# Performance work log

Hardware: AMD Instinct MI355X
Metric: run time of the kernel (lower is better)

## Reference

```python
import jax, jax.numpy as jnp
import numpy as np

SEQ, BATCH, D_IN, D_H, RANK, D_OUT = 512, 128, 256, 1024, 128, 256


def setup_inputs() -> dict:
    key = jax.random.key(0)
    ks = jax.random.split(key, 7)
    s = 1.0 / np.sqrt(D_H)
    return {
        "x": jax.random.normal(ks[0], (SEQ, BATCH, D_IN), jnp.float32),
        "W_in": jax.random.normal(ks[1], (D_H, D_IN), jnp.float32) * (1.0 / np.sqrt(D_IN)),
        "U": jax.random.uniform(ks[2], (RANK, D_H), jnp.float32, -s, s),
        "V": jax.random.uniform(ks[3], (D_H, RANK), jnp.float32, -s, s),
        "b_h": jax.random.uniform(ks[4], (D_H,), jnp.float32, -s, s),
        "W_out": jax.random.normal(ks[5], (D_OUT, D_H), jnp.float32) * (1.0 / np.sqrt(D_H)),
        "b_out": jax.random.uniform(ks[6], (D_OUT,), jnp.float32, -s, s),
    }


def reference(x, W_in, U, V, b_h, W_out, b_out):
    # Precompute input projection for all timesteps: i2h has no bias (bias=0).
    zi = jnp.einsum('tbi,hi->tbh', x, W_in)  # [T,B,H]

    def step(h, zi_t):
        # low-rank h2h: h @ (V@U)^T + b_h == (h @ U^T) @ V^T + b_h
        zh = (h @ U.T) @ V.T + b_h
        h_new = jax.nn.relu(zh + zi_t)
        return h_new, h_new

    h0 = jnp.zeros((x.shape[1], V.shape[0]), x.dtype)
    _, hidden = jax.lax.scan(step, h0, zi)  # [T,B,H]
    output = hidden @ W_out.T + b_out       # [T,B,O]; output_activation=None -> identity
    return hidden, output
```

## Files before the change

### kernel.cpp

```cpp
#include <hip/hip_runtime.h>

typedef __bf16 bf16;
typedef __bf16 bf16x4 __attribute__((ext_vector_type(4)));
typedef __bf16 bf16x8 __attribute__((ext_vector_type(8)));
typedef float  f32x4  __attribute__((ext_vector_type(4)));
typedef unsigned long long u64;

#define MFMA(a,b,c) __builtin_amdgcn_mfma_f32_16x16x32_bf16((a),(b),(c),0,0,0)

#define TSTEPS 512
#define NBATCH 128
#define DIN    256
#define DH     1024
#define NRANK  128
#define DOUT   256

#define NBG 8
#define NGH 4

#define ZI_OFF    0ull
#define QSEQ_OFF  134217728ull
#define PBUF_OFF  150994944ull
#define FLAG_OFF  (PBUF_OFF + 262144ull)
#define WIN_OFF   151519232ull
#define U_OFF     152043520ull
#define V_OFF     152305664ull
#define WOUT_OFF  152567808ull
#define BAR_OFF   153092096ull

__device__ __forceinline__ void cstore64(u64* p, u64 v) {
  __hip_atomic_store(p, v, __ATOMIC_RELAXED, __HIP_MEMORY_SCOPE_AGENT);
}
__device__ __forceinline__ u64 cload64(const u64* p) {
  return __hip_atomic_load(p, __ATOMIC_RELAXED, __HIP_MEMORY_SCOPE_AGENT);
}
union B4U { u64 u; bf16x4 b; };

__global__ __launch_bounds__(256) void k_prep(const float* __restrict__ W_in,
                                              const float* __restrict__ U,
                                              const float* __restrict__ V,
                                              const float* __restrict__ W_out,
                                              char* __restrict__ ws) {
  bf16* winb  = (bf16*)(ws + WIN_OFF);
  bf16* ub    = (bf16*)(ws + U_OFF);
  bf16* vb    = (bf16*)(ws + V_OFF);
  bf16* woutb = (bf16*)(ws + WOUT_OFF);
  bf16* qseq  = (bf16*)(ws + QSEQ_OFF);
  unsigned* flg = (unsigned*)(ws + FLAG_OFF);
  size_t id = (size_t)blockIdx.x * 256 + threadIdx.x;
  if      (id < 262144) winb[id]           = (bf16)W_in[id];
  else if (id < 393216) ub[id - 262144]    = (bf16)U[id - 262144];
  else if (id < 524288) vb[id - 393216]    = (bf16)V[id - 393216];
  else if (id < 786432) woutb[id - 524288] = (bf16)W_out[id - 524288];
  else if (id < 802816) qseq[id - 786432]  = (bf16)0.0f;
  else if (id < 802848) flg[id - 802816]   = 0u;
}

__global__ __launch_bounds__(256) void k_zi(const float* __restrict__ x,
                                            const char* __restrict__ ws,
                                            bf16* __restrict__ zi) {
  const bf16* winb = (const bf16*)(ws + WIN_OFF);
  __shared__ bf16 xl[128 * 264];
  __shared__ bf16 wl[128 * 264];
  const int tid = threadIdx.x, lane = tid & 63, wv = tid >> 6;
  const int q4 = lane >> 4, l16 = lane & 15;
  const int m0b = blockIdx.x * 128, n0 = blockIdx.y * 128;

  for (int ch = tid; ch < 8192; ch += 256) {
    int r = ch >> 6, c4 = ch & 63;
    float4 f = *(const float4*)&x[(size_t)(m0b + r) * 256 + c4 * 4];
    bf16x4 b; b[0] = (bf16)f.x; b[1] = (bf16)f.y; b[2] = (bf16)f.z; b[3] = (bf16)f.w;
    *(bf16x4*)&xl[r * 264 + c4 * 4] = b;
  }
  for (int ch = tid; ch < 4096; ch += 256) {
    int r = ch >> 5, c8 = ch & 31;
    *(uint4*)&wl[r * 264 + c8 * 8] = *(const uint4*)&winb[(size_t)(n0 + r) * 256 + c8 * 8];
  }
  __syncthreads();

  f32x4 z4 = {0.f, 0.f, 0.f, 0.f};
  f32x4 acc[2][8];
#pragma unroll
  for (int i = 0; i < 2; i++)
#pragma unroll
    for (int j = 0; j < 8; j++) acc[i][j] = z4;

  const int m0 = wv * 32;
#pragma unroll
  for (int kc = 0; kc < 8; kc++) {
    bf16x8 a0 = *(bf16x8*)&xl[(m0 + l16) * 264 + kc * 32 + q4 * 8];
    bf16x8 a1 = *(bf16x8*)&xl[(m0 + 16 + l16) * 264 + kc * 32 + q4 * 8];
#pragma unroll
    for (int nt = 0; nt < 8; nt++) {
      bf16x8 b = *(bf16x8*)&wl[(nt * 16 + l16) * 264 + kc * 32 + q4 * 8];
      acc[0][nt] = MFMA(a0, b, acc[0][nt]);
      acc[1][nt] = MFMA(a1, b, acc[1][nt]);
    }
  }
  __syncthreads();
#pragma unroll
  for (int mt = 0; mt < 2; mt++)
#pragma unroll
    for (int nt = 0; nt < 8; nt++)
#pragma unroll
      for (int r = 0; r < 4; r++) {
        int m = m0 + mt * 16 + q4 * 4 + r;
        int c = nt * 16 + l16;
        xl[m * 136 + c] = (bf16)acc[mt][nt][r];
      }
  __syncthreads();
  for (int ch = tid; ch < 2048; ch += 256) {
    int r = ch >> 4, c8 = ch & 15;
    *(uint4*)&zi[(size_t)(m0b + r) * 1024 + n0 + c8 * 8] = *(uint4*)&xl[r * 136 + c8 * 8];
  }
}

__global__ __launch_bounds__(256) void k_scan(char* __restrict__ ws,
                                              const float* __restrict__ b_h) {
  const bf16* zi = (const bf16*)(ws + ZI_OFF);
  const bf16* ub = (const bf16*)(ws + U_OFF);
  const bf16* vb = (const bf16*)(ws + V_OFF);
  bf16* qseq = (bf16*)(ws + QSEQ_OFF);
  u64* pbufq = (u64*)(ws + PBUF_OFF);
  unsigned* flag = (unsigned*)(ws + FLAG_OFF);

  __shared__ bf16 Vl[256 * 136];
  __shared__ bf16 Ul[128 * 264];
  __shared__ bf16 ql[16 * 136];
  __shared__ bf16 hl[16 * 264];
  __shared__ bf16 ps[16 * 136];

  const int tid = threadIdx.x, lane = tid & 63, w = tid >> 6;
  const int l16 = lane & 15, q4 = lane >> 4;
  const int bg = blockIdx.x & 7, g = blockIdx.x >> 3;
  const int brow0 = bg * 16, hcol0 = g * 256;

  for (int ch = tid; ch < 4096; ch += 256) {
    int r = ch >> 4, c8 = ch & 15;
    *(uint4*)&Vl[r * 136 + c8 * 8] = *(const uint4*)&vb[(size_t)(hcol0 + r) * 128 + c8 * 8];
  }
  for (int ch = tid; ch < 4096; ch += 256) {
    int r = ch >> 5, c8 = ch & 31;
    *(uint4*)&Ul[r * 264 + c8 * 8] = *(const uint4*)&ub[(size_t)r * 1024 + hcol0 + c8 * 8];
  }
  for (int i = tid; i < 16 * 136; i += 256) ql[i] = (bf16)0.0f;

  float bj[4];
#pragma unroll
  for (int nt = 0; nt < 4; nt++) bj[nt] = b_h[hcol0 + w * 64 + nt * 16 + l16];

  bf16 zcur[16], znxt[16];
#pragma unroll
  for (int nt = 0; nt < 4; nt++)
#pragma unroll
    for (int rr = 0; rr < 4; rr++)
      zcur[nt * 4 + rr] = zi[(size_t)(brow0 + q4 * 4 + rr) * 1024 + hcol0 + w * 64 + nt * 16 + l16];
  __syncthreads();

  const f32x4 z4 = {0.f, 0.f, 0.f, 0.f};

  for (int t = 0; t < TSTEPS - 1; t++) {
    f32x4 az[4] = {z4, z4, z4, z4};
#pragma unroll
    for (int kc = 0; kc < 4; kc++) {
      bf16x8 a = *(const bf16x8*)&ql[l16 * 136 + kc * 32 + q4 * 8];
#pragma unroll
      for (int nt = 0; nt < 4; nt++) {
        bf16x8 bb = *(const bf16x8*)&Vl[(w * 64 + nt * 16 + l16) * 136 + kc * 32 + q4 * 8];
        az[nt] = MFMA(a, bb, az[nt]);
      }
    }
#pragma unroll
    for (int nt = 0; nt < 4; nt++)
#pragma unroll
      for (int rr = 0; rr < 4; rr++) {
        float v = az[nt][rr] + bj[nt] + (float)zcur[nt * 4 + rr];
        hl[(q4 * 4 + rr) * 264 + w * 64 + nt * 16 + l16] = (bf16)fmaxf(v, 0.0f);
      }
    __syncthreads();

    f32x4 ap[2] = {z4, z4};
#pragma unroll
    for (int kc = 0; kc < 8; kc++) {
      bf16x8 a = *(const bf16x8*)&hl[l16 * 264 + kc * 32 + q4 * 8];
#pragma unroll
      for (int nt = 0; nt < 2; nt++) {
        bf16x8 bb = *(const bf16x8*)&Ul[(w * 32 + nt * 16 + l16) * 264 + kc * 32 + q4 * 8];
        ap[nt] = MFMA(a, bb, ap[nt]);
      }
    }
#pragma unroll
    for (int nt = 0; nt < 2; nt++)
#pragma unroll
      for (int rr = 0; rr < 4; rr++)
        ps[(q4 * 4 + rr) * 136 + w * 32 + nt * 16 + l16] = (bf16)ap[nt][rr];
    __syncthreads();

    const int par = t & 1;
    u64* mybuf = &pbufq[(size_t)((par * NBG + bg) * NGH + g) * 512];
#pragma unroll
    for (int i = 0; i < 2; i++) {
      int e = tid + i * 256;
      int r = e >> 5, c4 = e & 31;
      cstore64(&mybuf[e], *(const u64*)&ps[r * 136 + c4 * 4]);
    }
    __syncthreads();
    if (tid == 0)
      __hip_atomic_store(&flag[bg * 4 + g], (unsigned)(t + 1), __ATOMIC_RELEASE, __HIP_MEMORY_SCOPE_AGENT);

#pragma unroll
    for (int nt = 0; nt < 4; nt++)
#pragma unroll
      for (int rr = 0; rr < 4; rr++)
        znxt[nt * 4 + rr] =
            zi[((size_t)(t + 1) * NBATCH + brow0 + q4 * 4 + rr) * 1024 + hcol0 + w * 64 + nt * 16 + l16];

    if (tid < NGH) {
      while (__hip_atomic_load(&flag[bg * 4 + tid], __ATOMIC_RELAXED, __HIP_MEMORY_SCOPE_AGENT) <
             (unsigned)(t + 1)) {}
    }
    __syncthreads();

    const u64* base = &pbufq[(size_t)(par * NBG + bg) * NGH * 512];
#pragma unroll
    for (int i = 0; i < 2; i++) {
      int e = tid + i * 256;
      int r = e >> 5, c4 = e & 31;
      float s0 = 0.f, s1 = 0.f, s2 = 0.f, s3 = 0.f;
#pragma unroll
      for (int p = 0; p < NGH; p++) {
        B4U v; v.u = cload64(&base[(size_t)p * 512 + e]);
        s0 += (float)v.b[0]; s1 += (float)v.b[1]; s2 += (float)v.b[2]; s3 += (float)v.b[3];
      }
      B4U o; o.b[0] = (bf16)s0; o.b[1] = (bf16)s1; o.b[2] = (bf16)s2; o.b[3] = (bf16)s3;
      *(bf16x4*)&ql[r * 136 + c4 * 4] = o.b;
      if (g == 0)
        *(u64*)&qseq[((size_t)(t + 1) * NBATCH + brow0 + r) * 128 + c4 * 4] = o.u;
    }
    __syncthreads();
#pragma unroll
    for (int k = 0; k < 16; k++) zcur[k] = znxt[k];
  }
}

__global__ __launch_bounds__(256) void k_hidden(const char* __restrict__ ws,
                                                const float* __restrict__ b_h,
                                                float* __restrict__ hid) {
  const bf16* qseq = (const bf16*)(ws + QSEQ_OFF);
  const bf16* vb   = (const bf16*)(ws + V_OFF);
  const bf16* zi   = (const bf16*)(ws + ZI_OFF);
  const int t = blockIdx.x, n0 = blockIdx.y * 128;
  const int tid = threadIdx.x, lane = tid & 63, wv = tid >> 6;
  const int q4 = lane >> 4, l16 = lane & 15;

  __shared__ bf16 ql2[128 * 136];
  __shared__ bf16 vl2[128 * 136];
  __shared__ bf16 zl2[128 * 136];
  __shared__ float bl2[128];

  for (int ch = tid; ch < 2048; ch += 256) {
    int r = ch >> 4, c8 = ch & 15;
    *(uint4*)&ql2[r * 136 + c8 * 8] = *(const uint4*)&qseq[(size_t)t * 16384 + r * 128 + c8 * 8];
    *(uint4*)&vl2[r * 136 + c8 * 8] = *(const uint4*)&vb[(size_t)(n0 + r) * 128 + c8 * 8];
    *(uint4*)&zl2[r * 136 + c8 * 8] = *(const uint4*)&zi[((size_t)t * 128 + r) * 1024 + n0 + c8 * 8];
  }
  if (tid < 128) bl2[tid] = b_h[n0 + tid];
  __syncthreads();

  f32x4 z4 = {0.f, 0.f, 0.f, 0.f};
  f32x4 acc[2][8];
#pragma unroll
  for (int i = 0; i < 2; i++)
#pragma unroll
    for (int j = 0; j < 8; j++) acc[i][j] = z4;

  const int m0 = wv * 32;
#pragma unroll
  for (int kc = 0; kc < 4; kc++) {
    bf16x8 a0 = *(bf16x8*)&ql2[(m0 + l16) * 136 + kc * 32 + q4 * 8];
    bf16x8 a1 = *(bf16x8*)&ql2[(m0 + 16 + l16) * 136 + kc * 32 + q4 * 8];
#pragma unroll
    for (int nt = 0; nt < 8; nt++) {
      bf16x8 b = *(bf16x8*)&vl2[(nt * 16 + l16) * 136 + kc * 32 + q4 * 8];
      acc[0][nt] = MFMA(a0, b, acc[0][nt]);
      acc[1][nt] = MFMA(a1, b, acc[1][nt]);
    }
  }
#pragma unroll
  for (int mt = 0; mt < 2; mt++)
#pragma unroll
    for (int nt = 0; nt < 8; nt++)
#pragma unroll
      for (int r = 0; r < 4; r++) {
        int m = m0 + mt * 16 + q4 * 4 + r;
        int c = nt * 16 + l16;
        float v = acc[mt][nt][r] + bl2[c] + (float)zl2[m * 136 + c];
        hid[((size_t)t * 128 + m) * 1024 + n0 + c] = fmaxf(v, 0.0f);
      }
}

__global__ __launch_bounds__(512) void k_out(const char* __restrict__ ws,
                                             const float* __restrict__ hid,
                                             const float* __restrict__ b_out,
                                             float* __restrict__ out) {
  const bf16* woutb = (const bf16*)(ws + WOUT_OFF);
  const int t = blockIdx.x;
  const int tid = threadIdx.x, lane = tid & 63, wv = tid >> 6;
  const int q4 = lane >> 4, l16 = lane & 15;

  __shared__ bf16 hl2[128 * 136];
  __shared__ bf16 wl2[256 * 136];
  __shared__ float bol[256];
  if (tid < 256) bol[tid] = b_out[tid];

  f32x4 z4 = {0.f, 0.f, 0.f, 0.f};
  f32x4 acc[16];
#pragma unroll
  for (int j = 0; j < 16; j++) acc[j] = z4;

  const int m0 = wv * 16;
  for (int k0 = 0; k0 < 1024; k0 += 128) {
    __syncthreads();
    for (int ch = tid; ch < 4096; ch += 512) {
      int r = ch >> 5, c4 = ch & 31;
      float4 f = *(const float4*)&hid[((size_t)t * 128 + r) * 1024 + k0 + c4 * 4];
      bf16x4 b; b[0] = (bf16)f.x; b[1] = (bf16)f.y; b[2] = (bf16)f.z; b[3] = (bf16)f.w;
      *(bf16x4*)&hl2[r * 136 + c4 * 4] = b;
    }
    for (int ch = tid; ch < 4096; ch += 512) {
      int r = ch >> 4, c8 = ch & 15;
      *(uint4*)&wl2[r * 136 + c8 * 8] = *(const uint4*)&woutb[(size_t)r * 1024 + k0 + c8 * 8];
    }
    __syncthreads();
#pragma unroll
    for (int kc = 0; kc < 4; kc++) {
      bf16x8 a = *(bf16x8*)&hl2[(m0 + l16) * 136 + kc * 32 + q4 * 8];
#pragma unroll
      for (int nt = 0; nt < 16; nt++) {
        bf16x8 b = *(bf16x8*)&wl2[(nt * 16 + l16) * 136 + kc * 32 + q4 * 8];
        acc[nt] = MFMA(a, b, acc[nt]);
      }
    }
  }
#pragma unroll
  for (int nt = 0; nt < 16; nt++)
#pragma unroll
    for (int r = 0; r < 4; r++) {
      int m = m0 + q4 * 4 + r;
      int c = nt * 16 + l16;
      out[((size_t)t * 128 + m) * 256 + c] = acc[nt][r] + bol[c];
    }
}

extern "C" void kernel_launch(void* const* d_in, const int* in_sizes, int n_in,
                              void* d_out, int out_size, void* d_ws, size_t ws_size,
                              hipStream_t stream) {
  (void)in_sizes; (void)n_in; (void)out_size; (void)ws_size;
  const float* x     = (const float*)d_in[0];
  const float* W_in  = (const float*)d_in[1];
  const float* U     = (const float*)d_in[2];
  const float* V     = (const float*)d_in[3];
  const float* b_h   = (const float*)d_in[4];
  const float* W_out = (const float*)d_in[5];
  const float* b_out = (const float*)d_in[6];
  char* ws = (char*)d_ws;
  float* hid = (float*)d_out;
  float* out = hid + (size_t)TSTEPS * NBATCH * DH;
  bf16* zi = (bf16*)(ws + ZI_OFF);

  k_prep<<<dim3(3137), dim3(256), 0, stream>>>(W_in, U, V, W_out, ws);
  k_zi<<<dim3(512, 8), dim3(256), 0, stream>>>(x, ws, zi);
  k_scan<<<dim3(NBG * NGH), dim3(256), 0, stream>>>(ws, b_h);
  k_hidden<<<dim3(512, 8), dim3(256), 0, stream>>>(ws, b_h, hid);
  k_out<<<dim3(512), dim3(512), 0, stream>>>(ws, hid, b_out, out);
}
```

Measured before the change: 2.505 ms.

## Interleave two batch groups per scan block and keep U/V weights in registers

The recurrent scan now runs 16 blocks instead of 32. Each block handles two 16-row batch groups and alternates between them, so one group's cross-block partial-sum exchange and wait overlap with the other group's compute. The V and U weight fragments move from LDS into registers. The block's own partial is read from LDS instead of global memory, and the next zi load is issued earlier. The costs are heavy register pressure and half as many CUs doing serial work per step.

```diff
diff --git a/kernel.cpp b/kernel.cpp
--- a/kernel.cpp
+++ b/kernel.cpp
@@ -15,8 +15,8 @@
 #define NRANK  128
 #define DOUT   256
 
-#define NBG 8
-#define NGH 4
+#define NPAIR 4
+#define NGH   4
 
 #define ZI_OFF    0ull
 #define QSEQ_OFF  134217728ull
@@ -115,8 +115,8 @@
   }
 }
 
-__global__ __launch_bounds__(256) void k_scan(char* __restrict__ ws,
-                                              const float* __restrict__ b_h) {
+__global__ __launch_bounds__(256, 1) void k_scan(char* __restrict__ ws,
+                                                 const float* __restrict__ b_h) {
   const bf16* zi = (const bf16*)(ws + ZI_OFF);
   const bf16* ub = (const bf16*)(ws + U_OFF);
   const bf16* vb = (const bf16*)(ws + V_OFF);
@@ -124,122 +124,136 @@
   u64* pbufq = (u64*)(ws + PBUF_OFF);
   unsigned* flag = (unsigned*)(ws + FLAG_OFF);
 
-  __shared__ bf16 Vl[256 * 136];
-  __shared__ bf16 Ul[128 * 264];
-  __shared__ bf16 ql[16 * 136];
-  __shared__ bf16 hl[16 * 264];
-  __shared__ bf16 ps[16 * 136];
+  __shared__ bf16 qA[16 * 136], qB[16 * 136];
+  __shared__ bf16 hA[16 * 264], hB[16 * 264];
+  __shared__ bf16 psA[16 * 136], psB[16 * 136];
 
   const int tid = threadIdx.x, lane = tid & 63, w = tid >> 6;
   const int l16 = lane & 15, q4 = lane >> 4;
-  const int bg = blockIdx.x & 7, g = blockIdx.x >> 3;
-  const int brow0 = bg * 16, hcol0 = g * 256;
-
-  for (int ch = tid; ch < 4096; ch += 256) {
-    int r = ch >> 4, c8 = ch & 15;
-    *(uint4*)&Vl[r * 136 + c8 * 8] = *(const uint4*)&vb[(size_t)(hcol0 + r) * 128 + c8 * 8];
-  }
-  for (int ch = tid; ch < 4096; ch += 256) {
-    int r = ch >> 5, c8 = ch & 31;
-    *(uint4*)&Ul[r * 264 + c8 * 8] = *(const uint4*)&ub[(size_t)r * 1024 + hcol0 + c8 * 8];
-  }
-  for (int i = tid; i < 16 * 136; i += 256) ql[i] = (bf16)0.0f;
+  const int p = blockIdx.x & 3, g = blockIdx.x >> 2;
+  const int hcol0 = g * 256;
+  const int rowA = p * 32, rowB = p * 32 + 16;
+
+  bf16x8 Vf[4][4];
+  bf16x8 Uf[8][2];
+#pragma unroll
+  for (int kc = 0; kc < 4; kc++)
+#pragma unroll
+    for (int nt = 0; nt < 4; nt++)
+      Vf[kc][nt] = *(const bf16x8*)&vb[(size_t)(hcol0 + w * 64 + nt * 16 + l16) * 128 + kc * 32 + q4 * 8];
+#pragma unroll
+  for (int kc = 0; kc < 8; kc++)
+#pragma unroll
+    for (int nt = 0; nt < 2; nt++)
+      Uf[kc][nt] = *(const bf16x8*)&ub[(size_t)(w * 32 + nt * 16 + l16) * 1024 + hcol0 + kc * 32 + q4 * 8];
 
   float bj[4];
 #pragma unroll
   for (int nt = 0; nt < 4; nt++) bj[nt] = b_h[hcol0 + w * 64 + nt * 16 + l16];
 
-  bf16 zcur[16], znxt[16];
+  for (int i = tid; i < 16 * 136; i += 256) { qA[i] = (bf16)0.0f; qB[i] = (bf16)0.0f; }
+
+  bf16 zA[16], zB[16];
 #pragma unroll
   for (int nt = 0; nt < 4; nt++)
 #pragma unroll
-    for (int rr = 0; rr < 4; rr++)
-      zcur[nt * 4 + rr] = zi[(size_t)(brow0 + q4 * 4 + rr) * 1024 + hcol0 + w * 64 + nt * 16 + l16];
+    for (int rr = 0; rr < 4; rr++) {
+      int c = hcol0 + w * 64 + nt * 16 + l16;
+      zA[nt * 4 + rr] = zi[(size_t)(rowA + q4 * 4 + rr) * 1024 + c];
+      zB[nt * 4 + rr] = zi[(size_t)(rowB + q4 * 4 + rr) * 1024 + c];
+    }
   __syncthreads();
 
   const f32x4 z4 = {0.f, 0.f, 0.f, 0.f};
 
-  for (int t = 0; t < TSTEPS - 1; t++) {
+  auto COMP = [&](int t, int half, bf16* qX, bf16* hX, bf16* psX, bf16 (&zX)[16], int row0) {
     f32x4 az[4] = {z4, z4, z4, z4};
 #pragma unroll
     for (int kc = 0; kc < 4; kc++) {
-      bf16x8 a = *(const bf16x8*)&ql[l16 * 136 + kc * 32 + q4 * 8];
-#pragma unroll
-      for (int nt = 0; nt < 4; nt++) {
-        bf16x8 bb = *(const bf16x8*)&Vl[(w * 64 + nt * 16 + l16) * 136 + kc * 32 + q4 * 8];
-        az[nt] = MFMA(a, bb, az[nt]);
-      }
+      bf16x8 a = *(const bf16x8*)&qX[l16 * 136 + kc * 32 + q4 * 8];
+#pragma unroll
+      for (int nt = 0; nt < 4; nt++) az[nt] = MFMA(a, Vf[kc][nt], az[nt]);
     }
 #pragma unroll
     for (int nt = 0; nt < 4; nt++)
 #pragma unroll
       for (int rr = 0; rr < 4; rr++) {
-        float v = az[nt][rr] + bj[nt] + (float)zcur[nt * 4 + rr];
-        hl[(q4 * 4 + rr) * 264 + w * 64 + nt * 16 + l16] = (bf16)fmaxf(v, 0.0f);
-      }
-    __syncthreads();
-
-    f32x4 ap[2] = {z4, z4};
-#pragma unroll
-    for (int kc = 0; kc < 8; kc++) {
-      bf16x8 a = *(const bf16x8*)&hl[l16 * 264 + kc * 32 + q4 * 8];
+        float v = az[nt][rr] + bj[nt] + (float)zX[nt * 4 + rr];
+        hX[(q4 * 4 + rr) * 264 + w * 64 + nt * 16 + l16] = (bf16)fmaxf(v, 0.0f);
+      }
+    __syncthreads();
+#pragma unroll
+    for (int nt = 0; nt < 4; nt++)
+#pragma unroll
+      for (int rr = 0; rr < 4; rr++)
+        zX[nt * 4 + rr] =
+            zi[((size_t)(t + 1) * NBATCH + row0 + q4 * 4 + rr) * 1024 + hcol0 + w * 64 + nt * 16 + l16];
+    f32x4 ap0[2] = {z4, z4}, ap1[2] = {z4, z4};
+#pragma unroll
+    for (int kc = 0; kc < 8; kc += 2) {
+      bf16x8 a0 = *(const bf16x8*)&hX[l16 * 264 + kc * 32 + q4 * 8];
+      bf16x8 a1 = *(const bf16x8*)&hX[l16 * 264 + (kc + 1) * 32 + q4 * 8];
 #pragma unroll
       for (int nt = 0; nt < 2; nt++) {
-        bf16x8 bb = *(const bf16x8*)&Ul[(w * 32 + nt * 16 + l16) * 264 + kc * 32 + q4 * 8];
-        ap[nt] = MFMA(a, bb, ap[nt]);
-      }
-    }
-#pragma unroll
-    for (int nt = 0; nt < 2; nt++)
+        ap0[nt] = MFMA(a0, Uf[kc][nt], ap0[nt]);
+        ap1[nt] = MFMA(a1, Uf[kc + 1][nt], ap1[nt]);
+      }
+    }
+#pragma unroll
+    for (int nt = 0; nt < 2; nt++) {
+      f32x4 s = ap0[nt] + ap1[nt];
 #pragma unroll
       for (int rr = 0; rr < 4; rr++)
-        ps[(q4 * 4 + rr) * 136 + w * 32 + nt * 16 + l16] = (bf16)ap[nt][rr];
-    __syncthreads();
-
-    const int par = t & 1;
-    u64* mybuf = &pbufq[(size_t)((par * NBG + bg) * NGH + g) * 512];
+        psX[(q4 * 4 + rr) * 136 + w * 32 + nt * 16 + l16] = (bf16)s[rr];
+    }
+    __syncthreads();
+    u64* mybuf = &pbufq[(size_t)(((((t + 1) & 1) * 2 + half) * NPAIR + p) * NGH + g) * 512];
 #pragma unroll
     for (int i = 0; i < 2; i++) {
       int e = tid + i * 256;
-      int r = e >> 5, c4 = e & 31;
-      cstore64(&mybuf[e], *(const u64*)&ps[r * 136 + c4 * 4]);
+      cstore64(&mybuf[e], *(const u64*)&psX[(e >> 5) * 136 + (e & 31) * 4]);
     }
     __syncthreads();
     if (tid == 0)
-      __hip_atomic_store(&flag[bg * 4 + g], (unsigned)(t + 1), __ATOMIC_RELEASE, __HIP_MEMORY_SCOPE_AGENT);
-
-#pragma unroll
-    for (int nt = 0; nt < 4; nt++)
-#pragma unroll
-      for (int rr = 0; rr < 4; rr++)
-        znxt[nt * 4 + rr] =
-            zi[((size_t)(t + 1) * NBATCH + brow0 + q4 * 4 + rr) * 1024 + hcol0 + w * 64 + nt * 16 + l16];
-
+      __hip_atomic_store(&flag[(half * NPAIR + p) * NGH + g], (unsigned)(t + 1),
+                         __ATOMIC_RELEASE, __HIP_MEMORY_SCOPE_AGENT);
+  };
+
+  auto PR = [&](int t, int half, bf16* qX, bf16* psX, int row0) {
     if (tid < NGH) {
-      while (__hip_atomic_load(&flag[bg * 4 + tid], __ATOMIC_RELAXED, __HIP_MEMORY_SCOPE_AGENT) <
-             (unsigned)(t + 1)) {}
-    }
-    __syncthreads();
-
-    const u64* base = &pbufq[(size_t)(par * NBG + bg) * NGH * 512];
+      while (__hip_atomic_load(&flag[(half * NPAIR + p) * NGH + tid],
+                               __ATOMIC_RELAXED, __HIP_MEMORY_SCOPE_AGENT) < (unsigned)t) {}
+    }
+    __syncthreads();
+    const u64* base = &pbufq[(size_t)(((t & 1) * 2 + half) * NPAIR + p) * NGH * 512];
 #pragma unroll
     for (int i = 0; i < 2; i++) {
       int e = tid + i * 256;
       int r = e >> 5, c4 = e & 31;
       float s0 = 0.f, s1 = 0.f, s2 = 0.f, s3 = 0.f;
 #pragma unroll
-      for (int p = 0; p < NGH; p++) {
-        B4U v; v.u = cload64(&base[(size_t)p * 512 + e]);
+      for (int pp = 0; pp < NGH; pp++) {
+        B4U v;
+        if (pp == g) v.u = *(const u64*)&psX[r * 136 + c4 * 4];
+        else         v.u = cload64(&base[(size_t)pp * 512 + e]);
         s0 += (float)v.b[0]; s1 += (float)v.b[1]; s2 += (float)v.b[2]; s3 += (float)v.b[3];
       }
       B4U o; o.b[0] = (bf16)s0; o.b[1] = (bf16)s1; o.b[2] = (bf16)s2; o.b[3] = (bf16)s3;
-      *(bf16x4*)&ql[r * 136 + c4 * 4] = o.b;
+      *(bf16x4*)&qX[r * 136 + c4 * 4] = o.b;
       if (g == 0)
-        *(u64*)&qseq[((size_t)(t + 1) * NBATCH + brow0 + r) * 128 + c4 * 4] = o.u;
-    }
-    __syncthreads();
-#pragma unroll
-    for (int k = 0; k < 16; k++) zcur[k] = znxt[k];
+        *(u64*)&qseq[((size_t)t * NBATCH + row0 + r) * NRANK + c4 * 4] = o.u;
+    }
+    __syncthreads();
+  };
+
+  COMP(0, 0, qA, hA, psA, zA, rowA);
+  COMP(0, 1, qB, hB, psB, zB, rowB);
+
+  for (int t = 1; t < TSTEPS; t++) {
+    PR(t, 0, qA, psA, rowA);
+    if (t < TSTEPS - 1) COMP(t, 0, qA, hA, psA, zA, rowA);
+    PR(t, 1, qB, psB, rowB);
+    if (t < TSTEPS - 1) COMP(t, 1, qB, hB, psB, zB, rowB);
   }
 }
 
@@ -370,7 +384,7 @@
 
   k_prep<<<dim3(3137), dim3(256), 0, stream>>>(W_in, U, V, W_out, ws);
   k_zi<<<dim3(512, 8), dim3(256), 0, stream>>>(x, ws, zi);
-  k_scan<<<dim3(NBG * NGH), dim3(256), 0, stream>>>(ws, b_h);
+  k_scan<<<dim3(NPAIR * NGH), dim3(256), 0, stream>>>(ws, b_h);
   k_hidden<<<dim3(512, 8), dim3(256), 0, stream>>>(ws, b_h, hid);
   k_out<<<dim3(512), dim3(512), 0, stream>>>(ws, hid, b_out, out);
 }
```

Result: slower. 3.867 ms (+54.4%).

## Replace flag-based cross-block exchange with tagged-value polling in scan

Applied to the files above, without the earlier changes.

The recurrent scan's cross-block partial-sum exchange now embeds the timestep tag alongside each packed bf16 pair in a 64-bit word. Consumers poll the data words directly, which removes the separate release flag, the LDS staging buffer and several block barriers per step. The MFMA operands are swapped so each lane writes its results straight to global memory, the next-step zi prefetch moves to the top of the loop, and the remaining barriers wait only on LDS. The exchange buffer reuses the W_in workspace region, so a new clear kernel zeroes it before the scan. The tag scheme relies on each 64-bit store and load being atomic, and every thread now spins on its own loads.

```diff
diff --git a/kernel.cpp b/kernel.cpp
--- a/kernel.cpp
+++ b/kernel.cpp
@@ -5,6 +5,7 @@
 typedef __bf16 bf16x8 __attribute__((ext_vector_type(8)));
 typedef float  f32x4  __attribute__((ext_vector_type(4)));
 typedef unsigned long long u64;
+typedef unsigned int u32;
 
 #define MFMA(a,b,c) __builtin_amdgcn_mfma_f32_16x16x32_bf16((a),(b),(c),0,0,0)
 
@@ -34,7 +35,13 @@
 __device__ __forceinline__ u64 cload64(const u64* p) {
   return __hip_atomic_load(p, __ATOMIC_RELAXED, __HIP_MEMORY_SCOPE_AGENT);
 }
-union B4U { u64 u; bf16x4 b; };
+
+#define BAR_LGKM() do { \
+  asm volatile("s_waitcnt lgkmcnt(0)" ::: "memory"); \
+  __builtin_amdgcn_sched_barrier(0); \
+  __builtin_amdgcn_s_barrier(); \
+  __builtin_amdgcn_sched_barrier(0); \
+} while (0)
 
 __global__ __launch_bounds__(256) void k_prep(const float* __restrict__ W_in,
                                               const float* __restrict__ U,
@@ -115,20 +122,23 @@
   }
 }
 
+__global__ __launch_bounds__(256) void k_clr(char* __restrict__ ws) {
+  u64* tp = (u64*)(ws + WIN_OFF);
+  tp[(size_t)blockIdx.x * 256 + threadIdx.x] = 0ull;
+}
+
 __global__ __launch_bounds__(256) void k_scan(char* __restrict__ ws,
                                               const float* __restrict__ b_h) {
   const bf16* zi = (const bf16*)(ws + ZI_OFF);
   const bf16* ub = (const bf16*)(ws + U_OFF);
   const bf16* vb = (const bf16*)(ws + V_OFF);
   bf16* qseq = (bf16*)(ws + QSEQ_OFF);
-  u64* pbufq = (u64*)(ws + PBUF_OFF);
-  unsigned* flag = (unsigned*)(ws + FLAG_OFF);
+  u64* tpb = (u64*)(ws + WIN_OFF);
 
   __shared__ bf16 Vl[256 * 136];
   __shared__ bf16 Ul[128 * 264];
   __shared__ bf16 ql[16 * 136];
   __shared__ bf16 hl[16 * 264];
-  __shared__ bf16 ps[16 * 136];
 
   const int tid = threadIdx.x, lane = tid & 63, w = tid >> 6;
   const int l16 = lane & 15, q4 = lane >> 4;
@@ -158,8 +168,19 @@
   __syncthreads();
 
   const f32x4 z4 = {0.f, 0.f, 0.f, 0.f};
+  const int rrow = tid >> 4, rk0 = (tid & 15) * 8;
 
   for (int t = 0; t < TSTEPS - 1; t++) {
+    const u32 tg = (u32)(t + 1);
+    const int par = (t + 1) & 1;
+
+#pragma unroll
+    for (int nt = 0; nt < 4; nt++)
+#pragma unroll
+      for (int rr = 0; rr < 4; rr++)
+        znxt[nt * 4 + rr] =
+            zi[((size_t)(t + 1) * NBATCH + brow0 + q4 * 4 + rr) * 1024 + hcol0 + w * 64 + nt * 16 + l16];
+
     f32x4 az[4] = {z4, z4, z4, z4};
 #pragma unroll
     for (int kc = 0; kc < 4; kc++) {
@@ -177,67 +198,63 @@
         float v = az[nt][rr] + bj[nt] + (float)zcur[nt * 4 + rr];
         hl[(q4 * 4 + rr) * 264 + w * 64 + nt * 16 + l16] = (bf16)fmaxf(v, 0.0f);
       }
-    __syncthreads();
+    BAR_LGKM();
 
     f32x4 ap[2] = {z4, z4};
 #pragma unroll
     for (int kc = 0; kc < 8; kc++) {
-      bf16x8 a = *(const bf16x8*)&hl[l16 * 264 + kc * 32 + q4 * 8];
-#pragma unroll
-      for (int nt = 0; nt < 2; nt++) {
-        bf16x8 bb = *(const bf16x8*)&Ul[(w * 32 + nt * 16 + l16) * 264 + kc * 32 + q4 * 8];
-        ap[nt] = MFMA(a, bb, ap[nt]);
-      }
-    }
-#pragma unroll
-    for (int nt = 0; nt < 2; nt++)
-#pragma unroll
-      for (int rr = 0; rr < 4; rr++)
-        ps[(q4 * 4 + rr) * 136 + w * 32 + nt * 16 + l16] = (bf16)ap[nt][rr];
-    __syncthreads();
-
-    const int par = t & 1;
-    u64* mybuf = &pbufq[(size_t)((par * NBG + bg) * NGH + g) * 512];
-#pragma unroll
-    for (int i = 0; i < 2; i++) {
-      int e = tid + i * 256;
-      int r = e >> 5, c4 = e & 31;
-      cstore64(&mybuf[e], *(const u64*)&ps[r * 136 + c4 * 4]);
-    }
-    __syncthreads();
-    if (tid == 0)
-      __hip_atomic_store(&flag[bg * 4 + g], (unsigned)(t + 1), __ATOMIC_RELEASE, __HIP_MEMORY_SCOPE_AGENT);
-
-#pragma unroll
-    for (int nt = 0; nt < 4; nt++)
-#pragma unroll
-      for (int rr = 0; rr < 4; rr++)
-        znxt[nt * 4 + rr] =
-            zi[((size_t)(t + 1) * NBATCH + brow0 + q4 * 4 + rr) * 1024 + hcol0 + w * 64 + nt * 16 + l16];
-
-    if (tid < NGH) {
-      while (__hip_atomic_load(&flag[bg * 4 + tid], __ATOMIC_RELAXED, __HIP_MEMORY_SCOPE_AGENT) <
-             (unsigned)(t + 1)) {}
-    }
-    __syncthreads();
-
-    const u64* base = &pbufq[(size_t)(par * NBG + bg) * NGH * 512];
-#pragma unroll
-    for (int i = 0; i < 2; i++) {
-      int e = tid + i * 256;
-      int r = e >> 5, c4 = e & 31;
-      float s0 = 0.f, s1 = 0.f, s2 = 0.f, s3 = 0.f;
-#pragma unroll
-      for (int p = 0; p < NGH; p++) {
-        B4U v; v.u = cload64(&base[(size_t)p * 512 + e]);
-        s0 += (float)v.b[0]; s1 += (float)v.b[1]; s2 += (float)v.b[2]; s3 += (float)v.b[3];
-      }
-      B4U o; o.b[0] = (bf16)s0; o.b[1] = (bf16)s1; o.b[2] = (bf16)s2; o.b[3] = (bf16)s3;
-      *(bf16x4*)&ql[r * 136 + c4 * 4] = o.b;
-      if (g == 0)
-        *(u64*)&qseq[((size_t)(t + 1) * NBATCH + brow0 + r) * 128 + c4 * 4] = o.u;
-    }
-    __syncthreads();
+      bf16x8 bh = *(const bf16x8*)&hl[l16 * 264 + kc * 32 + q4 * 8];
+#pragma unroll
+      for (int mt = 0; mt < 2; mt++) {
+        bf16x8 au = *(const bf16x8*)&Ul[(w * 32 + mt * 16 + l16) * 264 + kc * 32 + q4 * 8];
+        ap[mt] = MFMA(au, bh, ap[mt]);
+      }
+    }
+
+    u64* myp = &tpb[(size_t)((par * NBG + bg) * NGH + g) * 1024];
+#pragma unroll
+    for (int mt = 0; mt < 2; mt++) {
+      u32 b0 = (u32)__builtin_bit_cast(unsigned short, (bf16)ap[mt][0]);
+      u32 b1 = (u32)__builtin_bit_cast(unsigned short, (bf16)ap[mt][1]);
+      u32 b2 = (u32)__builtin_bit_cast(unsigned short, (bf16)ap[mt][2]);
+      u32 b3 = (u32)__builtin_bit_cast(unsigned short, (bf16)ap[mt][3]);
+      int e0 = l16 * 64 + w * 16 + mt * 8 + q4 * 2;
+      cstore64(&myp[e0],     ((u64)((b1 << 16) | b0) << 32) | tg);
+      cstore64(&myp[e0 + 1], ((u64)((b3 << 16) | b2) << 32) | tg);
+    }
+
+    const u64* rb = &tpb[(size_t)(par * NBG + bg) * NGH * 1024];
+    u64 vv[4][4];
+#pragma unroll
+    for (int p4 = 0; p4 < 4; p4++)
+#pragma unroll
+      for (int i = 0; i < 4; i++)
+        vv[p4][i] = cload64(&rb[(size_t)p4 * 1024 + tid * 4 + i]);
+#pragma unroll
+    for (int p4 = 0; p4 < 4; p4++)
+#pragma unroll
+      for (int i = 0; i < 4; i++)
+        while ((u32)vv[p4][i] != tg) vv[p4][i] = cload64(&rb[(size_t)p4 * 1024 + tid * 4 + i]);
+
+    float s[8] = {0.f, 0.f, 0.f, 0.f, 0.f, 0.f, 0.f, 0.f};
+#pragma unroll
+    for (int p4 = 0; p4 < 4; p4++)
+#pragma unroll
+      for (int i = 0; i < 4; i++) {
+        u32 hi = (u32)(vv[p4][i] >> 32);
+        s[2 * i]     += __builtin_bit_cast(float, (hi & 0xFFFFu) << 16);
+        s[2 * i + 1] += __builtin_bit_cast(float, (hi >> 16) << 16);
+      }
+
+    union { bf16x8 v; uint4 u; } qv;
+#pragma unroll
+    for (int k = 0; k < 8; k++) qv.v[k] = (bf16)s[k];
+    *(bf16x8*)&ql[rrow * 136 + rk0] = qv.v;
+    if (g == 0)
+      *(uint4*)&qseq[((size_t)(t + 1) * NBATCH + brow0 + rrow) * NRANK + rk0] = qv.u;
+
+    BAR_LGKM();
+
 #pragma unroll
     for (int k = 0; k < 16; k++) zcur[k] = znxt[k];
   }
@@ -370,6 +387,7 @@
 
   k_prep<<<dim3(3137), dim3(256), 0, stream>>>(W_in, U, V, W_out, ws);
   k_zi<<<dim3(512, 8), dim3(256), 0, stream>>>(x, ws, zi);
+  k_clr<<<dim3(256), dim3(256), 0, stream>>>(ws);
   k_scan<<<dim3(NBG * NGH), dim3(256), 0, stream>>>(ws, b_h);
   k_hidden<<<dim3(512, 8), dim3(256), 0, stream>>>(ws, b_h, hid);
   k_out<<<dim3(512), dim3(512), 0, stream>>>(ws, hid, b_out, out);
```

After: 3.799 ms. +51.6%, slower.
